# Kernel tuning notes

Measured on AMD Instinct MI355X. Metric: run time of the kernel, lower is better.

## Reference

```python
import jax, jax.numpy as jnp
import numpy as np

NUM_VARS = 256
NUM_NODES = 65536
NUM_CATS = 256
BATCH = 512


def setup_inputs() -> dict:
    key = jax.random.key(0)
    k1, k2, k3 = jax.random.split(key, 3)
    # data: [num_vars, batch] categorical observations
    data = jax.random.randint(k1, (NUM_VARS, BATCH), 0, NUM_CATS, dtype=jnp.int64)
    # params: flat [num_nodes * num_cats] categorical probabilities (positive)
    params = jax.random.uniform(k2, (NUM_NODES * NUM_CATS,), dtype=jnp.float32, minval=0.01, maxval=1.0)
    # vids: per-node variable id (scope), irregular assignment
    vids = jax.random.randint(k3, (NUM_NODES,), 0, NUM_VARS, dtype=jnp.int64)
    # s_pids: per-node parameter start offset (untied, contiguous: node n owns params[n*num_cats : (n+1)*num_cats])
    s_pids = jnp.arange(NUM_NODES, dtype=jnp.int64) * NUM_CATS
    return {"data": data, "params": params, "vids": vids, "s_pids": s_pids}


def reference(data, params, vids, s_pids):
    # Gather the observed category of each node's variable: [num_nodes, batch]
    dvals = data[vids]                      # irregular gather over vars
    pidx = s_pids[:, None] + dvals          # per-node param index [N, B]
    mars = jnp.log(params[pidx])            # fw_mar_fn for Categorical: log p[node, cat]
    return mars                             # node_mars[node_offset:node_offset+N, :]
```

## Files before the change

### kernel.cpp

```cpp
#include <hip/hip_runtime.h>

#define NUM_VARS  256
#define NUM_NODES 65536
#define NUM_CATS  256
#define BATCH     512
#define NODES_PER_BLOCK 8

typedef __attribute__((ext_vector_type(4))) float f32x4;
typedef __attribute__((ext_vector_type(4))) int   i32x4;

__global__ __launch_bounds__(256) void input_layer_kernel(
    const int*   __restrict__ data,
    const float* __restrict__ params,
    const int*   __restrict__ vids,
    const int*   __restrict__ s_pids,
    float*       __restrict__ out)
{
    __shared__ float logp[NODES_PER_BLOCK * NUM_CATS];
    const int t  = threadIdx.x;
    const int gb = blockIdx.x * NODES_PER_BLOCK;

#pragma unroll
    for (int h = 0; h < 2; ++h) {
        const int r = (t >> 6) + h * 4;
        const int c = (t & 63) * 4;
        const int spid = s_pids[gb + r];
        const f32x4 p = __builtin_nontemporal_load(
            reinterpret_cast<const f32x4*>(&params[spid + c]));
        f32x4 lp;
        lp.x = __logf(p.x); lp.y = __logf(p.y);
        lp.z = __logf(p.z); lp.w = __logf(p.w);
        *reinterpret_cast<f32x4*>(&logp[r * NUM_CATS + c]) = lp;
    }
    __syncthreads();

#pragma unroll
    for (int ch = 0; ch < 4; ++ch) {
        const int e = ch * 1024 + t * 4;
        const int k = e >> 9;
        const int b = e & (BATCH - 1);
        const int vid = vids[gb + k];
        const i32x4 dv = *reinterpret_cast<const i32x4*>(&data[vid * BATCH + b]);
        f32x4 r;
        r.x = logp[k * NUM_CATS + dv.x];
        r.y = logp[k * NUM_CATS + dv.y];
        r.z = logp[k * NUM_CATS + dv.z];
        r.w = logp[k * NUM_CATS + dv.w];
        __builtin_nontemporal_store(r,
            reinterpret_cast<f32x4*>(&out[(gb + k) * BATCH + b]));
    }
}

extern "C" void kernel_launch(void* const* d_in, const int* in_sizes, int n_in,
                              void* d_out, int out_size, void* d_ws, size_t ws_size,
                              hipStream_t stream) {
    const int*   data   = (const int*)d_in[0];
    const float* params = (const float*)d_in[1];
    const int*   vids   = (const int*)d_in[2];
    const int*   s_pids = (const int*)d_in[3];
    float*       out    = (float*)d_out;

    const int block = 256;
    const int grid  = NUM_NODES / NODES_PER_BLOCK;
    input_layer_kernel<<<grid, block, 0, stream>>>(data, params, vids, s_pids, out);
}
```

Before: 39.23 us.

## Give each wave its own nodes, dropping block barrier and batching loads

Each wavefront now owns four nodes end-to-end, so it builds and reads only its own LDS rows and the block-wide __syncthreads is removed. All params and data loads for the wave are issued up front (node ids made wave-uniform via readfirstlane) to overlap memory latency, and nodes per block go up to 16 with a min-blocks launch bound. The trade-off is higher register pressure from holding many vector loads in flight, and twice the LDS per block.

```diff
diff --git a/kernel.cpp b/kernel.cpp
--- a/kernel.cpp
+++ b/kernel.cpp
@@ -4,12 +4,13 @@
 #define NUM_NODES 65536
 #define NUM_CATS  256
 #define BATCH     512
-#define NODES_PER_BLOCK 8
+#define NODES_PER_WAVE  4
+#define NODES_PER_BLOCK 16
 
 typedef __attribute__((ext_vector_type(4))) float f32x4;
 typedef __attribute__((ext_vector_type(4))) int   i32x4;
 
-__global__ __launch_bounds__(256) void input_layer_kernel(
+__global__ __launch_bounds__(256, 8) void input_layer_kernel(
     const int*   __restrict__ data,
     const float* __restrict__ params,
     const int*   __restrict__ vids,
@@ -17,37 +18,56 @@
     float*       __restrict__ out)
 {
     __shared__ float logp[NODES_PER_BLOCK * NUM_CATS];
-    const int t  = threadIdx.x;
-    const int gb = blockIdx.x * NODES_PER_BLOCK;
+    const int t    = threadIdx.x;
+    const int w    = t >> 6;
+    const int lane = t & 63;
+    const int c    = lane * 4;
+    const int gb   = blockIdx.x * NODES_PER_BLOCK;
+    const int nb   = gb + NODES_PER_WAVE * w;
+
+    float* const rows = &logp[NODES_PER_WAVE * w * NUM_CATS];
+
+    int spid[NODES_PER_WAVE], vid[NODES_PER_WAVE];
+#pragma unroll
+    for (int j = 0; j < NODES_PER_WAVE; ++j) {
+        spid[j] = __builtin_amdgcn_readfirstlane(s_pids[nb + j]);
+        vid[j]  = __builtin_amdgcn_readfirstlane(vids[nb + j]);
+    }
+
+    f32x4 p[NODES_PER_WAVE];
+#pragma unroll
+    for (int j = 0; j < NODES_PER_WAVE; ++j)
+        p[j] = __builtin_nontemporal_load(
+            reinterpret_cast<const f32x4*>(&params[spid[j] + c]));
+
+    i32x4 dv[2 * NODES_PER_WAVE];
+#pragma unroll
+    for (int j = 0; j < NODES_PER_WAVE; ++j) {
+#pragma unroll
+        for (int h = 0; h < 2; ++h)
+            dv[2 * j + h] = *reinterpret_cast<const i32x4*>(
+                &data[vid[j] * BATCH + h * 256 + c]);
+    }
 
 #pragma unroll
-    for (int h = 0; h < 2; ++h) {
-        const int r = (t >> 6) + h * 4;
-        const int c = (t & 63) * 4;
-        const int spid = s_pids[gb + r];
-        const f32x4 p = __builtin_nontemporal_load(
-            reinterpret_cast<const f32x4*>(&params[spid + c]));
-        f32x4 lp;
-        lp.x = __logf(p.x); lp.y = __logf(p.y);
-        lp.z = __logf(p.z); lp.w = __logf(p.w);
-        *reinterpret_cast<f32x4*>(&logp[r * NUM_CATS + c]) = lp;
+    for (int j = 0; j < NODES_PER_WAVE; ++j) {
+        f32x4 l;
+        l.x = __logf(p[j].x); l.y = __logf(p[j].y);
+        l.z = __logf(p[j].z); l.w = __logf(p[j].w);
+        *reinterpret_cast<f32x4*>(&rows[j * NUM_CATS + c]) = l;
     }
-    __syncthreads();
 
 #pragma unroll
-    for (int ch = 0; ch < 4; ++ch) {
-        const int e = ch * 1024 + t * 4;
-        const int k = e >> 9;
-        const int b = e & (BATCH - 1);
-        const int vid = vids[gb + k];
-        const i32x4 dv = *reinterpret_cast<const i32x4*>(&data[vid * BATCH + b]);
-        f32x4 r;
-        r.x = logp[k * NUM_CATS + dv.x];
-        r.y = logp[k * NUM_CATS + dv.y];
-        r.z = logp[k * NUM_CATS + dv.z];
-        r.w = logp[k * NUM_CATS + dv.w];
-        __builtin_nontemporal_store(r,
-            reinterpret_cast<f32x4*>(&out[(gb + k) * BATCH + b]));
+    for (int j = 0; j < NODES_PER_WAVE; ++j) {
+        const float* const row = &rows[j * NUM_CATS];
+#pragma unroll
+        for (int h = 0; h < 2; ++h) {
+            const i32x4 d = dv[2 * j + h];
+            f32x4 r;
+            r.x = row[d.x]; r.y = row[d.y]; r.z = row[d.z]; r.w = row[d.w];
+            __builtin_nontemporal_store(r, reinterpret_cast<f32x4*>(
+                &out[(nb + j) * BATCH + h * 256 + c]));
+        }
     }
 }
 
```

Result: slower. 42.57 us (+8.5%).
